# Optimization experiments

Hardware: AMD Instinct MI355X
Metric: run time of the kernel (lower is better)

## Reference

```python
import jax, jax.numpy as jnp
import numpy as np

TORSO_IDX = np.array([0, 1, 4, 7, 8, 11, 14])


def _nrm(v):
    return v / jnp.linalg.norm(v)


def _rod(v, k, theta):
    c = jnp.cos(theta)
    return c * v + (1.0 - c) * jnp.dot(v, k) * k + jnp.sin(theta) * jnp.cross(k, v)


def _per_sample(a, coord):
    cW = coord.reshape(-1, 3)  # (17, 3)
    torso = cW[TORSO_IDX]      # (7, 3)
    Y = torso[:, 2]
    X = jnp.stack([torso[:, 0], torso[:, 1], jnp.ones(7, dtype=coord.dtype)], axis=1)
    # least-squares plane fit: xt = (X^T X)^{-1} X^T Y
    xt = jnp.linalg.solve(X.T @ X, X.T @ Y)
    xt = xt.at[2].set(-1.0)
    yt = jnp.cross(cW[8] - cW[0], xt)
    zt = jnp.cross(xt, yt)
    xt, yt, zt = _nrm(xt), _nrm(yt), _nrm(zt)
    R = jnp.stack([xt, yt, zt], axis=0)  # R_TW (3,3)
    cT = cW @ R.T                        # torso-frame coords (17,3)

    x_T = jnp.array([1.0, 0.0, 0.0], dtype=coord.dtype)
    y_T = jnp.array([0.0, 1.0, 0.0], dtype=coord.dtype)
    z_T = jnp.array([0.0, 0.0, 1.0], dtype=coord.dtype)

    # head
    gt_0 = _nrm(cT[9] - cT[8])
    gt_1 = _nrm(jnp.cross(gt_0, jnp.cross(cT[10] - cT[9], -gt_0)))
    v_HP = _rod(z_T, y_T, a[0])
    v_HY_pre = _rod(x_T, y_T, a[0])
    v_HY = _rod(v_HY_pre, v_HP, a[1])
    # left arm
    gt_2 = _nrm(cT[12] - cT[11])
    gt_3 = _nrm(cT[13] - cT[12])
    v_LSP = _rod(x_T, y_T, a[3])
    v_LSR = _rod(v_LSP, _nrm(jnp.cross(cT[8] - cT[11], v_LSP)), a[4])
    v_LER = _rod(v_LSR, _nrm(jnp.cross(cT[8] - cT[11], v_LSR)), a[5])
    v_LEY = _rod(v_LER, v_LSR, a[6])
    # right arm
    gt_4 = _nrm(cT[15] - cT[14])
    gt_5 = _nrm(cT[16] - cT[15])
    v_RSP = _rod(x_T, y_T, a[6])
    v_RSR = _rod(v_RSP, _nrm(jnp.cross(v_RSP, cT[8] - cT[14])), a[7])
    v_RER = _rod(v_RSR, _nrm(jnp.cross(v_RSR, cT[8] - cT[14])), a[8])
    v_REY = _rod(v_RER, v_RSR, a[9])
    # left leg
    gt_6 = _nrm(cT[5] - cT[4])
    gt_7 = _nrm(cT[6] - cT[5])
    v_LHP = _rod(-z_T, y_T, a[10])
    k_LHR = _rod(x_T, y_T, a[10])
    k_LHYP = _rod(_nrm(jnp.array([0.0, 1.0, -1.0], dtype=coord.dtype)), y_T, a[10])
    v_LHR = _rod(v_LHP, k_LHR, a[11])
    k_LHYP = _rod(k_LHYP, k_LHR, a[11])
    v_LHYP = _rod(v_LHR, k_LHYP, a[12])
    v_LKP = _rod(v_LHYP, _nrm(jnp.cross(cT[6] - cT[5], -v_LHYP)), a[13])
    # right leg
    gt_8 = _nrm(cT[2] - cT[1])
    gt_9 = _nrm(cT[3] - cT[2])
    v_RHP = _rod(-z_T, y_T, a[14])
    k_RHR = _rod(x_T, y_T, a[14])
    k_RHYP = _rod(_nrm(jnp.array([0.0, 1.0, 1.0], dtype=coord.dtype)), y_T, a[14])
    v_RHR = _rod(v_RHP, k_RHR, a[15])
    k_RHYP = _rod(k_RHYP, k_RHR, a[15])
    v_RHYP = _rod(v_RHR, k_RHYP, a[16])
    v_RKP = _rod(v_RHYP, _nrm(jnp.cross(cT[3] - cT[2], -v_RHYP)), a[17])
    # ankles
    gt_rest = jnp.zeros(3, dtype=coord.dtype)
    k_LAP = _nrm(jnp.cross(cT[6] - cT[5], cT[4] - cT[5]))
    k_LAR = _nrm(jnp.cross(k_LAP, cT[5] - cT[6]))
    k_RAP = _nrm(jnp.cross(cT[3] - cT[2], cT[1] - cT[2]))
    k_RAR = _nrm(jnp.cross(k_RAP, cT[2] - cT[3]))
    k_LAP_W = k_LAP @ R
    k_LAR_W = k_LAR @ R
    k_RAP_W = k_RAP @ R
    k_RAR_W = k_RAR @ R
    v_LAP = _rod(k_LAR_W, k_LAP_W, a[18])
    v_LAR = _rod(k_LAP_W, v_LAP, a[19])
    v_RAP = _rod(k_RAR_W, k_RAP_W, a[20])
    v_RAR = _rod(k_RAP_W, v_RAP, a[21])
    v_LAP = v_LAP * z_T
    v_LAR = v_LAR * z_T
    v_RAP = v_RAP * z_T
    v_RAR = v_RAR * z_T

    gt = jnp.stack([gt_0, gt_1, gt_2, gt_3, gt_4, gt_5, gt_6, gt_7, gt_8, gt_9,
                    gt_rest, gt_rest, gt_rest, gt_rest], axis=0)
    sim = jnp.stack([v_HP, v_HY, v_LSR, v_LEY, v_RSR, v_REY, v_LHYP, v_LKP,
                     v_RHYP, v_RKP, v_LAP, v_LAR, v_RAP, v_RAR], axis=0)
    return jnp.mean((gt - sim) ** 2)


def setup_inputs() -> dict:
    key = jax.random.key(0)
    k1, k2 = jax.random.split(key)
    B = 524288
    angles = jax.random.normal(k1, (B, 22), dtype=jnp.float32)
    coordination = jax.random.normal(k2, (B, 51), dtype=jnp.float32)
    return {"angles": angles, "coordination": coordination}


def reference(angles, coordination):
    # mean over batch of per-sample MSE (sum of means / batch_size == mean)
    return jnp.mean(jax.vmap(_per_sample)(angles, coordination))
```

## Files before the change

### kernel.cpp

```cpp
#include <hip/hip_runtime.h>

struct F3 { float x, y, z; };
__device__ __forceinline__ F3 operator+(F3 a, F3 b){ return {a.x+b.x, a.y+b.y, a.z+b.z}; }
__device__ __forceinline__ F3 operator-(F3 a, F3 b){ return {a.x-b.x, a.y-b.y, a.z-b.z}; }
__device__ __forceinline__ F3 operator-(F3 a){ return {-a.x, -a.y, -a.z}; }
__device__ __forceinline__ F3 operator*(float s, F3 a){ return {s*a.x, s*a.y, s*a.z}; }
__device__ __forceinline__ float dot(F3 a, F3 b){ return a.x*b.x + a.y*b.y + a.z*b.z; }
__device__ __forceinline__ F3 cross(F3 a, F3 b){
  return { a.y*b.z - a.z*b.y, a.z*b.x - a.x*b.z, a.x*b.y - a.y*b.x };
}
__device__ __forceinline__ F3 nrm(F3 v){ float inv = rsqrtf(dot(v,v)); return inv*v; }
__device__ __forceinline__ float sq3(F3 v){ return dot(v,v); }
__device__ __forceinline__ F3 rod(F3 v, F3 k, float s, float c){
  float d = (1.0f - c) * dot(v, k);
  F3 cr = cross(k, v);
  return { c*v.x + d*k.x + s*cr.x,
           c*v.y + d*k.y + s*cr.y,
           c*v.z + d*k.z + s*cr.z };
}
__device__ __forceinline__ F3 mulR(F3 k, F3 rx, F3 ry, F3 rz){
  return { k.x*rx.x + k.y*ry.x + k.z*rz.x,
           k.x*rx.y + k.y*ry.y + k.z*rz.y,
           k.x*rx.z + k.y*ry.z + k.z*rz.z };
}

#define BLK 128

__global__ __launch_bounds__(BLK, 2)
void rodloss_kernel(const float* __restrict__ angles,
                    const float* __restrict__ coord,
                    double* __restrict__ acc)
{
  __shared__ __align__(16) float lds_a[BLK*22];
  __shared__ __align__(16) float lds_c[BLK*51];
  __shared__ float red[BLK/64];

  const int t = threadIdx.x;
  const long long base = (long long)blockIdx.x * BLK;

  {
    const float4* gA = (const float4*)(angles + base*22);
    float4* sA = (float4*)lds_a;
    #pragma unroll
    for (int i = 0; i < 6; ++i) {
      int idx = t + i*BLK;
      if (idx < (BLK*22/4)) sA[idx] = gA[idx];
    }
    const float4* gC = (const float4*)(coord + base*51);
    float4* sC = (float4*)lds_c;
    #pragma unroll
    for (int i = 0; i < 13; ++i) {
      int idx = t + i*BLK;
      if (idx < (BLK*51/4)) sC[idx] = gC[idx];
    }
  }
  __syncthreads();

  const float* A = &lds_a[t*22];
  const float* C = &lds_c[t*51];
  auto P = [&](int i) -> F3 { return { C[3*i], C[3*i+1], C[3*i+2] }; };

  float Sx=0.f,Sy=0.f,Sz=0.f,Sxx=0.f,Sxy=0.f,Syy=0.f,Sxz=0.f,Syz=0.f;
  {
    const int TIDX[7] = {0,1,4,7,8,11,14};
    #pragma unroll
    for (int i = 0; i < 7; ++i) {
      F3 p = P(TIDX[i]);
      Sx += p.x;  Sy += p.y;  Sz += p.z;
      Sxx += p.x*p.x;  Sxy += p.x*p.y;  Syy += p.y*p.y;
      Sxz += p.x*p.z;  Syz += p.y*p.z;
    }
  }
  const float a33 = 7.0f;
  float M00 = Syy*a33 - Sy*Sy;
  float M10 = Sxy*a33 - Sx*Sy;
  float M20 = Sxy*Sy  - Sx*Syy;
  float det  = Sxx*M00 - Sxy*M10 + Sx*M20;
  float detx = Sxz*M00 - Syz*M10 + Sz*M20;
  float dety = -Sxz*M10 + Syz*(Sxx*a33 - Sx*Sx) - Sz*(Sxx*Sy - Sx*Sxy);
  float invdet = 1.0f / det;

  F3 xtv = { detx*invdet, dety*invdet, -1.0f };
  F3 p0 = P(0), p8 = P(8);
  F3 ytv = cross(p8 - p0, xtv);
  F3 ztv = cross(xtv, ytv);
  F3 xt = nrm(xtv), yt = nrm(ytv), zt = nrm(ztv);

  auto T = [&](int i) -> F3 { F3 p = P(i); return { dot(xt,p), dot(yt,p), dot(zt,p) }; };

  const F3 X_T = {1.f,0.f,0.f}, Y_T = {0.f,1.f,0.f}, Z_T = {0.f,0.f,1.f};
  float L = 0.0f;

  F3 cT8 = T(8);

  {
    F3 cT9 = T(9), cT10 = T(10);
    F3 gt0 = nrm(cT9 - cT8);
    F3 gt1 = nrm(cross(gt0, cross(cT10 - cT9, -gt0)));
    float s0,c0; __sincosf(A[0], &s0, &c0);
    F3 v_HP = rod(Z_T, Y_T, s0, c0);
    F3 v_HY_pre = rod(X_T, Y_T, s0, c0);
    float s1,c1; __sincosf(A[1], &s1, &c1);
    F3 v_HY = rod(v_HY_pre, v_HP, s1, c1);
    L += sq3(gt0 - v_HP) + sq3(gt1 - v_HY);
  }

  float s6,c6; __sincosf(A[6], &s6, &c6);

  {
    F3 cT11 = T(11), cT12 = T(12), cT13 = T(13);
    F3 gt2 = nrm(cT12 - cT11);
    F3 gt3 = nrm(cT13 - cT12);
    F3 dL = cT8 - cT11;
    float s3,c3; __sincosf(A[3], &s3, &c3);
    F3 v_LSP = rod(X_T, Y_T, s3, c3);
    float s4,c4; __sincosf(A[4], &s4, &c4);
    F3 v_LSR = rod(v_LSP, nrm(cross(dL, v_LSP)), s4, c4);
    float s5,c5; __sincosf(A[5], &s5, &c5);
    F3 v_LER = rod(v_LSR, nrm(cross(dL, v_LSR)), s5, c5);
    F3 v_LEY = rod(v_LER, v_LSR, s6, c6);
    L += sq3(gt2 - v_LSR) + sq3(gt3 - v_LEY);
  }

  {
    F3 cT14 = T(14), cT15 = T(15), cT16 = T(16);
    F3 gt4 = nrm(cT15 - cT14);
    F3 gt5 = nrm(cT16 - cT15);
    F3 dR = cT8 - cT14;
    F3 v_RSP = rod(X_T, Y_T, s6, c6);
    float s7,c7; __sincosf(A[7], &s7, &c7);
    F3 v_RSR = rod(v_RSP, nrm(cross(v_RSP, dR)), s7, c7);
    float s8,c8; __sincosf(A[8], &s8, &c8);
    F3 v_RER = rod(v_RSR, nrm(cross(v_RSR, dR)), s8, c8);
    float s9,c9; __sincosf(A[9], &s9, &c9);
    F3 v_REY = rod(v_RER, v_RSR, s9, c9);
    L += sq3(gt4 - v_RSR) + sq3(gt5 - v_REY);
  }

  {
    F3 cT4 = T(4), cT5 = T(5), cT6 = T(6);
    F3 gt6 = nrm(cT5 - cT4);
    F3 gt7 = nrm(cT6 - cT5);
    float s10,c10; __sincosf(A[10], &s10, &c10);
    F3 v_LHP  = rod(-Z_T, Y_T, s10, c10);
    F3 k_LHR  = rod(X_T,  Y_T, s10, c10);
    const float r = 0.70710678118654752f;
    F3 k_LHYP = rod({0.f, r, -r}, Y_T, s10, c10);
    float s11,c11; __sincosf(A[11], &s11, &c11);
    F3 v_LHR = rod(v_LHP, k_LHR, s11, c11);
    k_LHYP   = rod(k_LHYP, k_LHR, s11, c11);
    float s12,c12; __sincosf(A[12], &s12, &c12);
    F3 v_LHYP = rod(v_LHR, k_LHYP, s12, c12);
    F3 d65 = cT6 - cT5;
    float s13,c13; __sincosf(A[13], &s13, &c13);
    F3 v_LKP = rod(v_LHYP, nrm(cross(d65, -v_LHYP)), s13, c13);
    L += sq3(gt6 - v_LHYP) + sq3(gt7 - v_LKP);
    F3 k_LAP = nrm(cross(d65, cT4 - cT5));
    F3 k_LAR = nrm(cross(k_LAP, cT5 - cT6));
    F3 k_LAP_W = mulR(k_LAP, xt, yt, zt);
    F3 k_LAR_W = mulR(k_LAR, xt, yt, zt);
    float s18,c18; __sincosf(A[18], &s18, &c18);
    F3 v_LAP = rod(k_LAR_W, k_LAP_W, s18, c18);
    float s19,c19; __sincosf(A[19], &s19, &c19);
    F3 v_LAR = rod(k_LAP_W, v_LAP, s19, c19);
    L += v_LAP.z*v_LAP.z + v_LAR.z*v_LAR.z;
  }

  {
    F3 cT1 = T(1), cT2 = T(2), cT3 = T(3);
    F3 gt8 = nrm(cT2 - cT1);
    F3 gt9 = nrm(cT3 - cT2);
    float s14,c14; __sincosf(A[14], &s14, &c14);
    F3 v_RHP  = rod(-Z_T, Y_T, s14, c14);
    F3 k_RHR  = rod(X_T,  Y_T, s14, c14);
    const float r = 0.70710678118654752f;
    F3 k_RHYP = rod({0.f, r, r}, Y_T, s14, c14);
    float s15,c15; __sincosf(A[15], &s15, &c15);
    F3 v_RHR = rod(v_RHP, k_RHR, s15, c15);
    k_RHYP   = rod(k_RHYP, k_RHR, s15, c15);
    float s16,c16; __sincosf(A[16], &s16, &c16);
    F3 v_RHYP = rod(v_RHR, k_RHYP, s16, c16);
    F3 d32 = cT3 - cT2;
    float s17,c17; __sincosf(A[17], &s17, &c17);
    F3 v_RKP = rod(v_RHYP, nrm(cross(d32, -v_RHYP)), s17, c17);
    L += sq3(gt8 - v_RHYP) + sq3(gt9 - v_RKP);
    F3 k_RAP = nrm(cross(d32, cT1 - cT2));
    F3 k_RAR = nrm(cross(k_RAP, cT2 - cT3));
    F3 k_RAP_W = mulR(k_RAP, xt, yt, zt);
    F3 k_RAR_W = mulR(k_RAR, xt, yt, zt);
    float s20,c20; __sincosf(A[20], &s20, &c20);
    F3 v_RAP = rod(k_RAR_W, k_RAP_W, s20, c20);
    float s21,c21; __sincosf(A[21], &s21, &c21);
    F3 v_RAR = rod(k_RAP_W, v_RAP, s21, c21);
    L += v_RAP.z*v_RAP.z + v_RAR.z*v_RAR.z;
  }

  float v = L;
  #pragma unroll
  for (int m = 32; m >= 1; m >>= 1) v += __shfl_xor(v, m, 64);
  if ((t & 63) == 0) red[t >> 6] = v;
  __syncthreads();
  if (t == 0) {
    float bs = red[0] + red[1];
    atomicAdd(acc, (double)bs);
  }
}

__global__ void finalize_kernel(const double* __restrict__ acc,
                                float* __restrict__ out, double scale)
{
  out[0] = (float)(acc[0] * scale);
}

extern "C" void kernel_launch(void* const* d_in, const int* in_sizes, int n_in,
                              void* d_out, int out_size, void* d_ws, size_t ws_size,
                              hipStream_t stream)
{
  const float* angles = (const float*)d_in[0];
  const float* coord  = (const float*)d_in[1];
  float* out = (float*)d_out;
  double* acc = (double*)d_ws;

  const int n  = in_sizes[0] / 22;
  const int nb = n / BLK;

  hipMemsetAsync(d_ws, 0, sizeof(double), stream);
  rodloss_kernel<<<nb, BLK, 0, stream>>>(angles, coord, acc);
  finalize_kernel<<<1, 1, 0, stream>>>(acc, out, 1.0 / (42.0 * (double)n));
}
```

Before: 220.4 us.

## Load angles directly to registers, shrink blocks, replace atomics with partial-sum reduction

Angles are now read straight from global memory into registers as float2 loads instead of being staged through LDS, which cuts LDS usage. Block size drops from 128 to 64 so more blocks can be resident. The double-precision atomicAdd per block and the memset are replaced by per-block float partials, summed by a separate 256-thread reduction kernel. The per-thread float2 loads use a 22-float stride, so they are less coalesced than the old staged float4 loads. The single-block reduction over 8192 partials adds a serial tail.

```diff
diff --git a/kernel.cpp b/kernel.cpp
--- a/kernel.cpp
+++ b/kernel.cpp
@@ -24,28 +24,19 @@
            k.x*rx.z + k.y*ry.z + k.z*rz.z };
 }
 
-#define BLK 128
-
-__global__ __launch_bounds__(BLK, 2)
+#define BLK 64
+
+__global__ __launch_bounds__(BLK, 3)
 void rodloss_kernel(const float* __restrict__ angles,
                     const float* __restrict__ coord,
-                    double* __restrict__ acc)
+                    float* __restrict__ partial)
 {
-  __shared__ __align__(16) float lds_a[BLK*22];
   __shared__ __align__(16) float lds_c[BLK*51];
-  __shared__ float red[BLK/64];
 
   const int t = threadIdx.x;
-  const long long base = (long long)blockIdx.x * BLK;
-
-  {
-    const float4* gA = (const float4*)(angles + base*22);
-    float4* sA = (float4*)lds_a;
-    #pragma unroll
-    for (int i = 0; i < 6; ++i) {
-      int idx = t + i*BLK;
-      if (idx < (BLK*22/4)) sA[idx] = gA[idx];
-    }
+  const size_t base = (size_t)blockIdx.x * BLK;
+
+  {
     const float4* gC = (const float4*)(coord + base*51);
     float4* sC = (float4*)lds_c;
     #pragma unroll
@@ -54,9 +45,18 @@
       if (idx < (BLK*51/4)) sC[idx] = gC[idx];
     }
   }
+
+  float A[22];
+  {
+    const float2* gA = (const float2*)(angles + (base + t) * 22);
+    #pragma unroll
+    for (int i = 0; i < 11; ++i) {
+      float2 v = gA[i];
+      A[2*i] = v.x; A[2*i+1] = v.y;
+    }
+  }
   __syncthreads();
 
-  const float* A = &lds_a[t*22];
   const float* C = &lds_c[t*51];
   auto P = [&](int i) -> F3 { return { C[3*i], C[3*i+1], C[3*i+2] }; };
 
@@ -198,18 +198,21 @@
   float v = L;
   #pragma unroll
   for (int m = 32; m >= 1; m >>= 1) v += __shfl_xor(v, m, 64);
-  if ((t & 63) == 0) red[t >> 6] = v;
+  if (t == 0) partial[blockIdx.x] = v;
+}
+
+__global__ void reduce_kernel(const float* __restrict__ part, int n,
+                              float* __restrict__ out, double scale)
+{
+  const int t = threadIdx.x;
+  double s = 0.0;
+  for (int i = t; i < n; i += 256) s += (double)part[i];
+  #pragma unroll
+  for (int m = 32; m >= 1; m >>= 1) s += __shfl_xor(s, m, 64);
+  __shared__ double red[4];
+  if ((t & 63) == 0) red[t >> 6] = s;
   __syncthreads();
-  if (t == 0) {
-    float bs = red[0] + red[1];
-    atomicAdd(acc, (double)bs);
-  }
-}
-
-__global__ void finalize_kernel(const double* __restrict__ acc,
-                                float* __restrict__ out, double scale)
-{
-  out[0] = (float)(acc[0] * scale);
+  if (t == 0) out[0] = (float)((red[0] + red[1] + red[2] + red[3]) * scale);
 }
 
 extern "C" void kernel_launch(void* const* d_in, const int* in_sizes, int n_in,
@@ -219,12 +222,11 @@
   const float* angles = (const float*)d_in[0];
   const float* coord  = (const float*)d_in[1];
   float* out = (float*)d_out;
-  double* acc = (double*)d_ws;
+  float* partial = (float*)d_ws;
 
   const int n  = in_sizes[0] / 22;
   const int nb = n / BLK;
 
-  hipMemsetAsync(d_ws, 0, sizeof(double), stream);
-  rodloss_kernel<<<nb, BLK, 0, stream>>>(angles, coord, acc);
-  finalize_kernel<<<1, 1, 0, stream>>>(acc, out, 1.0 / (42.0 * (double)n));
-}
+  rodloss_kernel<<<nb, BLK, 0, stream>>>(angles, coord, partial);
+  reduce_kernel<<<1, 256, 0, stream>>>(partial, nb, out, 1.0 / (42.0 * (double)n));
+}
```

New measurement: 201.9 us. 8.4% less time.
